# Performance work log

Hardware: AMD Instinct MI355X
Metric: run time of the kernel (lower is better)

The kernel has to match this reference:

```python
import jax, jax.numpy as jnp
import numpy as np

N_NODES = 100000


def gcn_conv(x, src, dst, W, b, num_nodes):
    # PyG GCNConv: add self-loops, symmetric normalization D^-1/2 (A+I) D^-1/2, then linear.
    loop = jnp.arange(num_nodes, dtype=src.dtype)
    s = jnp.concatenate([src, loop])
    d = jnp.concatenate([dst, loop])
    deg = jax.ops.segment_sum(jnp.ones_like(d, dtype=x.dtype), d, num_segments=num_nodes)
    dinv = jnp.where(deg > 0, jax.lax.rsqrt(deg), 0.0)
    norm = dinv[s] * dinv[d]                       # [E+N]
    h = x @ W                                      # [N, out]
    msg = h[s] * norm[:, None]                     # gather + scale
    out = jax.ops.segment_sum(msg, d, num_segments=num_nodes)  # scatter-add
    return out + b


def setup_inputs() -> dict:
    key = jax.random.key(0)
    k1, k2, k3, k4 = jax.random.split(key, 4)
    F_IN, HID, C = 165, 128, 2
    E = 3200000
    x = jax.random.normal(k1, (N_NODES, F_IN), dtype=jnp.float32)
    edge_index = jax.random.randint(k2, (2, E), 0, N_NODES, dtype=jnp.int64)
    W1 = jax.random.normal(k3, (F_IN, HID), dtype=jnp.float32) * (1.0 / np.sqrt(F_IN))
    b1 = jnp.zeros((HID,), dtype=jnp.float32)
    W2 = jax.random.normal(k4, (HID, C), dtype=jnp.float32) * (1.0 / np.sqrt(HID))
    b2 = jnp.zeros((C,), dtype=jnp.float32)
    return {"x": x, "edge_index": edge_index, "W1": W1, "b1": b1, "W2": W2, "b2": b2}


def reference(x, edge_index, W1, b1, W2, b2):
    src, dst = edge_index[0], edge_index[1]
    h = jax.nn.relu(gcn_conv(x, src, dst, W1, b1, N_NODES))
    # dropout is identity in eval mode (self.training=False)
    out = gcn_conv(h, src, dst, W2, b2, N_NODES)
    return out
```

## Files before the change

kernel.cpp:

```cpp
#include <hip/hip_runtime.h>

#define NN  100000
#define FIN 165
#define HID 128
#define NBUCK 391
#define CHUNK 8192
#define CAP   9216
#define KPAD 192
#define WS   196

typedef __attribute__((ext_vector_type(4))) float f32x4;
typedef __attribute__((ext_vector_type(8))) short short8;

#define OFF_DINV   0
#define OFF_H1     100352
#define OFF_Z      (OFF_H1 + NN * 64)
#define OFF_ROWPTR (OFF_Z + 2 * NN)
#define OFF_GBASE  (OFF_ROWPTR + 100352)
#define OFF_GCUR   (OFF_GBASE + 512)
#define OFF_BUCK   (OFF_GCUR + 512)
#define OFF_EDATA  (OFF_BUCK + NBUCK * CAP)
#define OFF_WTHI   (OFF_EDATA + 3200000)

__device__ __forceinline__ unsigned bf16rne(float f) {
    unsigned u = __float_as_uint(f);
    return (u + 0x7FFFu + ((u >> 16) & 1u)) >> 16;
}

__device__ __forceinline__ float2 bf2_to_f2(unsigned int u) {
    float2 r;
    r.x = __uint_as_float(u << 16);
    r.y = __uint_as_float(u & 0xffff0000u);
    return r;
}

__device__ __forceinline__ short8 ldfrag(const ushort* p) {
    union { uint2 u[2]; short8 s; } f;
    f.u[0] = *(const uint2*)p;
    f.u[1] = *(const uint2*)(p + 16);
    return f.s;
}

__global__ void k_wsplit(const float* __restrict__ W1, ushort* __restrict__ hi,
                         int* __restrict__ gcur) {
    int t = blockIdx.x * blockDim.x + threadIdx.x;
    if (t < 512) gcur[t] = t * CAP;
    if (t >= HID * KPAD) return;
    int ch = t / KPAD, k = t % KPAD;
    float v = (k < FIN) ? W1[k * HID + ch] : 0.0f;
    hi[ch * KPAD + k] = (ushort)bf16rne(v);
}

__global__ __launch_bounds__(1024) void k_bfill(const int* __restrict__ src,
        const int* __restrict__ dst, int* __restrict__ gcur,
        unsigned int* __restrict__ bucketed, int ne) {
    __shared__ int hist[NBUCK];
    __shared__ int lcur[NBUCK];
    for (int i = threadIdx.x; i < NBUCK; i += 1024) hist[i] = 0;
    __syncthreads();
    const int4* dst4 = (const int4*)dst;
    const int4* src4 = (const int4*)src;
    const int ne4 = ne >> 2;
    const int base4 = blockIdx.x * (CHUNK / 4);
#pragma unroll
    for (int it = 0; it < CHUNK / 4096; ++it) {
        int e4 = base4 + it * 1024 + threadIdx.x;
        if (e4 < ne4) {
            int4 v = dst4[e4];
            atomicAdd(&hist[v.x >> 8], 1);
            atomicAdd(&hist[v.y >> 8], 1);
            atomicAdd(&hist[v.z >> 8], 1);
            atomicAdd(&hist[v.w >> 8], 1);
        }
    }
    if (blockIdx.x == 0 && threadIdx.x < (ne & 3))
        atomicAdd(&hist[dst[(ne & ~3) + threadIdx.x] >> 8], 1);
    __syncthreads();
    for (int i = threadIdx.x; i < NBUCK; i += 1024) {
        int h = hist[i];
        lcur[i] = h ? atomicAdd(&gcur[i], h) : 0;
    }
    __syncthreads();
#define PUT(D, S)                                                            \
    {                                                                        \
        int b_ = (D) >> 8;                                                   \
        int pos_ = atomicAdd(&lcur[b_], 1);                                  \
        if (pos_ < (b_ + 1) * CAP)                                           \
            bucketed[pos_] = (unsigned)(S) | ((unsigned)((D) & 255) << 24);  \
    }
#pragma unroll
    for (int it = 0; it < CHUNK / 4096; ++it) {
        int e4 = base4 + it * 1024 + threadIdx.x;
        if (e4 < ne4) {
            int4 d4 = dst4[e4];
            int4 s4 = src4[e4];
            PUT(d4.x, s4.x);
            PUT(d4.y, s4.y);
            PUT(d4.z, s4.z);
            PUT(d4.w, s4.w);
        }
    }
    if (blockIdx.x == 0 && threadIdx.x < (ne & 3)) {
        int e = (ne & ~3) + threadIdx.x;
        PUT(dst[e], src[e]);
    }
#undef PUT
}

__global__ __launch_bounds__(512) void k_bscan(const int* __restrict__ gcur,
        int* __restrict__ gbase) {
    __shared__ int s[512];
    int tid = threadIdx.x;
    int c = 0;
    if (tid < NBUCK) {
        c = gcur[tid] - tid * CAP;
        c = min(c, CAP);
    }
    s[tid] = c;
    __syncthreads();
    for (int off = 1; off < 512; off <<= 1) {
        int t = (tid >= off) ? s[tid - off] : 0;
        __syncthreads();
        s[tid] += t;
        __syncthreads();
    }
    if (tid < NBUCK) gbase[tid] = s[tid] - c;
    if (tid == NBUCK - 1) gbase[NBUCK] = s[tid];
}

__global__ __launch_bounds__(512) void k_fused2(
        const float* __restrict__ x, const ushort* __restrict__ wthi,
        unsigned* __restrict__ h1, int n,
        const int* __restrict__ gbase, const unsigned int* __restrict__ bucketed,
        int* __restrict__ edata, int* __restrict__ rowptr,
        float* __restrict__ dinv) {
    __shared__ alignas(16) unsigned char smem[128 * WS * 2];

    if (blockIdx.x < NBUCK) {
        int* hist = (int*)smem;
        int* scan = hist + 256;
        int* lcur = scan + 256;
        const int b = blockIdx.x;
        const int tid = threadIdx.x;
        const int rbeg = b * CAP;
        const int wbeg = gbase[b], wend = gbase[b + 1];
        const int cnt = wend - wbeg;
        if (tid < 256) hist[tid] = 0;
        __syncthreads();
        for (int j = tid; j < cnt; j += 512)
            atomicAdd(&hist[bucketed[rbeg + j] >> 24], 1);
        __syncthreads();
        if (tid < 256) scan[tid] = hist[tid];
        __syncthreads();
        for (int off = 1; off < 256; off <<= 1) {
            int t = 0;
            if (tid < 256 && tid >= off) t = scan[tid - off];
            __syncthreads();
            if (tid < 256) scan[tid] += t;
            __syncthreads();
        }
        if (tid < 256) {
            int c = hist[tid];
            int excl = scan[tid] - c;
            int d = b * 256 + tid;
            if (d < n) {
                rowptr[d] = wbeg + excl;
                dinv[d] = rsqrtf((float)c + 1.0f);
            }
            lcur[tid] = wbeg + excl;
        }
        __syncthreads();
        for (int j = tid; j < cnt; j += 512) {
            unsigned p = bucketed[rbeg + j];
            int pos = atomicAdd(&lcur[p >> 24], 1);
            edata[pos] = (int)(p & 0x00FFFFFFu);
        }
        if (b == NBUCK - 1 && tid == 0) rowptr[n] = wend;
        return;
    }

    ushort* whi = (ushort*)smem;
    const int tid = threadIdx.x;
    const int node0 = (blockIdx.x - NBUCK) * 128;
    const int wv = tid >> 6, lane = tid & 63;
    const int r15 = lane & 15, g = lane >> 4;

    {
        int ch = tid >> 2, q = tid & 3;
        int gb = ch * KPAD + q * 48;
        int lb = ch * WS + q * 48;
#pragma unroll
        for (int j = 0; j < 12; ++j) {
            uint2 v = *(const uint2*)&wthi[gb + j * 4];
            *(uint2*)&whi[lb + j * 4] = v;
        }
    }

    const int row = node0 + wv * 16 + r15;
    const bool rowok = row < n;
    const float* xrow = x + (size_t)row * FIN;

    f32x4 acc[8];
#pragma unroll
    for (int ct = 0; ct < 8; ++ct) acc[ct] = (f32x4){0.f, 0.f, 0.f, 0.f};

    __syncthreads();

    for (int ks = 0; ks < 6; ++ks) {
        unsigned hh[8];
#pragma unroll
        for (int j = 0; j < 4; ++j) {
            int k0 = ks * 32 + 4 * g + j;
            int k1 = k0 + 16;
            float v0 = (rowok && k0 < FIN) ? xrow[k0] : 0.0f;
            float v1 = (rowok && k1 < FIN) ? xrow[k1] : 0.0f;
            hh[j]     = bf16rne(v0);
            hh[4 + j] = bf16rne(v1);
        }
        union { unsigned u[4]; short8 s; } A;
        A.u[0] = hh[0] | (hh[1] << 16);
        A.u[1] = hh[2] | (hh[3] << 16);
        A.u[2] = hh[4] | (hh[5] << 16);
        A.u[3] = hh[6] | (hh[7] << 16);
#pragma unroll
        for (int ct = 0; ct < 8; ++ct) {
            short8 Bh = ldfrag(&whi[(ct * 16 + r15) * WS + ks * 32 + 4 * g]);
            acc[ct] = __builtin_amdgcn_mfma_f32_16x16x32_bf16(A.s, Bh, acc[ct], 0, 0, 0);
        }
    }

#pragma unroll
    for (int ct = 0; ct < 4; ++ct) {
#pragma unroll
        for (int r = 0; r < 4; ++r) {
            int node = node0 + wv * 16 + 4 * g + r;
            if (node < n) {
                unsigned p = bf16rne(acc[ct][r]) | (bf16rne(acc[ct + 4][r]) << 16);
                h1[node * 64 + ct * 16 + r15] = p;
            }
        }
    }
}

__global__ __launch_bounds__(256) void k_agg_fused(const int* __restrict__ rowptr,
        const int* __restrict__ edata, const unsigned int* __restrict__ h1,
        const float* __restrict__ dinv, const float* __restrict__ b1,
        const float* __restrict__ W2, float* __restrict__ z, int n) {
    const int wid  = (blockIdx.x * blockDim.x + threadIdx.x) >> 6;
    const int lane = threadIdx.x & 63;
    if (wid >= n) return;
    const int d = wid;
    const int beg = rowptr[d], end = rowptr[d + 1];
    const float di = dinv[d];
    const int grp = lane >> 4;
    const int sl  = lane & 15;

    float ax0, ax1, ax2, ax3, ay0, ay1, ay2, ay3;
    {
        uint4 hv = *(const uint4*)&h1[d * 64 + sl * 4];
        float nm = (grp == 0) ? di * di : 0.0f;
        float2 f0 = bf2_to_f2(hv.x), f1 = bf2_to_f2(hv.y);
        float2 f2 = bf2_to_f2(hv.z), f3 = bf2_to_f2(hv.w);
        ax0 = f0.x * nm; ay0 = f0.y * nm;
        ax1 = f1.x * nm; ay1 = f1.y * nm;
        ax2 = f2.x * nm; ay2 = f2.y * nm;
        ax3 = f3.x * nm; ay3 = f3.y * nm;
    }

#define PRELOAD(JB)                                                          \
    {                                                                        \
        int i0 = (JB) + grp, i1 = (JB) + 4 + grp,                            \
            i2 = (JB) + 8 + grp, i3 = (JB) + 12 + grp;                       \
        int c0 = min(i0, end - 1), c1 = min(i1, end - 1);                    \
        int c2 = min(i2, end - 1), c3 = min(i3, end - 1);                    \
        s0 = edata[c0]; s1 = edata[c1]; s2 = edata[c2]; s3 = edata[c3];      \
        m0 = (i0 < end) ? dinv[s0] * di : 0.0f;                              \
        m1 = (i1 < end) ? dinv[s1] * di : 0.0f;                              \
        m2 = (i2 < end) ? dinv[s2] * di : 0.0f;                              \
        m3 = (i3 < end) ? dinv[s3] * di : 0.0f;                              \
    }
#define ACC(G, NM)                                                           \
    {                                                                        \
        float2 f;                                                            \
        f = bf2_to_f2((G).x); ax0 = fmaf(f.x, (NM), ax0); ay0 = fmaf(f.y, (NM), ay0); \
        f = bf2_to_f2((G).y); ax1 = fmaf(f.x, (NM), ax1); ay1 = fmaf(f.y, (NM), ay1); \
        f = bf2_to_f2((G).z); ax2 = fmaf(f.x, (NM), ax2); ay2 = fmaf(f.y, (NM), ay2); \
        f = bf2_to_f2((G).w); ax3 = fmaf(f.x, (NM), ax3); ay3 = fmaf(f.y, (NM), ay3); \
    }

    if (beg < end) {
        int s0, s1, s2, s3;
        float m0, m1, m2, m3;
        PRELOAD(beg);
        for (int j = beg; j < end; j += 16) {
            uint4 g0 = *(const uint4*)&h1[s0 * 64 + sl * 4];
            uint4 g1 = *(const uint4*)&h1[s1 * 64 + sl * 4];
            uint4 g2 = *(const uint4*)&h1[s2 * 64 + sl * 4];
            uint4 g3 = *(const uint4*)&h1[s3 * 64 + sl * 4];
            float w0 = m0, w1 = m1, w2 = m2, w3 = m3;
            int jn = j + 16;
            if (jn < end) PRELOAD(jn);
            ACC(g0, w0); ACC(g1, w1); ACC(g2, w2); ACC(g3, w3);
        }
    }
#undef PRELOAD
#undef ACC

    ax0 += __shfl_xor(ax0, 16, 64); ax0 += __shfl_xor(ax0, 32, 64);
    ax1 += __shfl_xor(ax1, 16, 64); ax1 += __shfl_xor(ax1, 32, 64);
    ax2 += __shfl_xor(ax2, 16, 64); ax2 += __shfl_xor(ax2, 32, 64);
    ax3 += __shfl_xor(ax3, 16, 64); ax3 += __shfl_xor(ax3, 32, 64);
    ay0 += __shfl_xor(ay0, 16, 64); ay0 += __shfl_xor(ay0, 32, 64);
    ay1 += __shfl_xor(ay1, 16, 64); ay1 += __shfl_xor(ay1, 32, 64);
    ay2 += __shfl_xor(ay2, 16, 64); ay2 += __shfl_xor(ay2, 32, 64);
    ay3 += __shfl_xor(ay3, 16, 64); ay3 += __shfl_xor(ay3, 32, 64);
    const int c = sl * 4;
    float4 bA = *(const float4*)&b1[c];
    float4 bB = *(const float4*)&b1[c + 64];
    float v00 = ax0 + bA.x; v00 = v00 > 0.f ? v00 : 0.f;
    float v01 = ax1 + bA.y; v01 = v01 > 0.f ? v01 : 0.f;
    float v02 = ax2 + bA.z; v02 = v02 > 0.f ? v02 : 0.f;
    float v03 = ax3 + bA.w; v03 = v03 > 0.f ? v03 : 0.f;
    float v10 = ay0 + bB.x; v10 = v10 > 0.f ? v10 : 0.f;
    float v11 = ay1 + bB.y; v11 = v11 > 0.f ? v11 : 0.f;
    float v12 = ay2 + bB.z; v12 = v12 > 0.f ? v12 : 0.f;
    float v13 = ay3 + bB.w; v13 = v13 > 0.f ? v13 : 0.f;
    float4 wA0 = *(const float4*)&W2[c * 2];
    float4 wA1 = *(const float4*)&W2[c * 2 + 4];
    float4 wB0 = *(const float4*)&W2[(c + 64) * 2];
    float4 wB1 = *(const float4*)&W2[(c + 64) * 2 + 4];
    float p0 = v00 * wA0.x + v01 * wA0.z + v02 * wA1.x + v03 * wA1.z
             + v10 * wB0.x + v11 * wB0.z + v12 * wB1.x + v13 * wB1.z;
    float p1 = v00 * wA0.y + v01 * wA0.w + v02 * wA1.y + v03 * wA1.w
             + v10 * wB0.y + v11 * wB0.w + v12 * wB1.y + v13 * wB1.w;
#pragma unroll
    for (int m = 8; m >= 1; m >>= 1) {
        p0 += __shfl_xor(p0, m, 64);
        p1 += __shfl_xor(p1, m, 64);
    }
    if (lane == 0) *(float2*)&z[d * 2] = make_float2(p0, p1);
}

__global__ __launch_bounds__(256) void k_out(const int* __restrict__ rowptr,
        const int* __restrict__ edata, const float* __restrict__ z,
        const float* __restrict__ dinv, const float* __restrict__ b2,
        float* __restrict__ out, int n) {
    int g = (blockIdx.x * blockDim.x + threadIdx.x) >> 4;
    int l = threadIdx.x & 15;
    if (g >= n) return;
    int beg = rowptr[g], end = rowptr[g + 1];
    float di = dinv[g];
    float o0 = 0.0f, o1 = 0.0f;
    for (int j = beg + l; j < end; j += 16) {
        int s = edata[j];
        float nm = dinv[s] * di;
        float2 zs = *(const float2*)&z[s * 2];
        o0 = fmaf(zs.x, nm, o0);
        o1 = fmaf(zs.y, nm, o1);
    }
#pragma unroll
    for (int m = 8; m >= 1; m >>= 1) {
        o0 += __shfl_xor(o0, m, 16);
        o1 += __shfl_xor(o1, m, 16);
    }
    if (l == 0) {
        float2 zd = *(const float2*)&z[g * 2];
        float s2 = di * di;
        out[g * 2]     = fmaf(zd.x, s2, b2[0]) + o0;
        out[g * 2 + 1] = fmaf(zd.y, s2, b2[1]) + o1;
    }
}

extern "C" void kernel_launch(void* const* d_in, const int* in_sizes, int n_in,
                              void* d_out, int out_size, void* d_ws, size_t ws_size,
                              hipStream_t stream) {
    const float* x  = (const float*)d_in[0];
    const int*   ei = (const int*)d_in[1];
    const float* W1 = (const float*)d_in[2];
    const float* b1 = (const float*)d_in[3];
    const float* W2 = (const float*)d_in[4];
    const float* b2 = (const float*)d_in[5];
    float* out = (float*)d_out;

    const int n  = in_sizes[0] / FIN;
    const int ne = in_sizes[1] / 2;
    const int* src = ei;
    const int* dst = ei + ne;

    float* ws     = (float*)d_ws;
    float* dinv   = ws + OFF_DINV;
    unsigned int* h1 = (unsigned int*)(ws + OFF_H1);
    float* z      = ws + OFF_Z;
    int*   rowptr = (int*)(ws + OFF_ROWPTR);
    int*   gbase  = (int*)(ws + OFF_GBASE);
    int*   gcur   = (int*)(ws + OFF_GCUR);
    unsigned int* bucketed = (unsigned int*)(ws + OFF_BUCK);
    int*   edata  = (int*)(ws + OFF_EDATA);
    ushort* wthi  = (ushort*)(ws + OFF_WTHI);

    const int nchb  = (ne + CHUNK - 1) / CHUNK;
    const int ngemm = (n + 127) / 128;

    k_wsplit<<<(HID * KPAD + 255) / 256, 256, 0, stream>>>(W1, wthi, gcur);
    k_bfill<<<nchb, 1024, 0, stream>>>(src, dst, gcur, bucketed, ne);
    k_bscan<<<1, 512, 0, stream>>>(gcur, gbase);
    k_fused2<<<NBUCK + ngemm, 512, 0, stream>>>(x, wthi, h1, n,
                                                gbase, bucketed, edata, rowptr, dinv);
    k_agg_fused<<<((size_t)n * 64 + 255) / 256, 256, 0, stream>>>(
        rowptr, edata, h1, dinv, b1, W2, z, n);
    k_out<<<(n * 16 + 255) / 256, 256, 0, stream>>>(rowptr, edata, z, dinv, b2, out, n);
}
```

Before: 227.5 us.

## Drop bucket scan kernel, use per-bucket padded CSR and deeper gather prefetch

Removes the single-block bucket prefix-scan kernel by keeping edges in padded per-bucket regions and storing separate row begin and end arrays, so the CSR build no longer needs a global scan or one extra launch. The bucket-fill kernel now uses a fixed count of 256 persistent blocks that each loop over a contiguous slice, which cuts global atomics on the bucket cursors. The layer-1 aggregation gathers 32 neighbours per iteration instead of 16, giving more loads in flight per wave. The costs are a larger edata buffer, extra row-end reads, and more registers in the aggregation kernel.

```diff
diff --git a/kernel.cpp b/kernel.cpp
--- a/kernel.cpp
+++ b/kernel.cpp
@@ -4,10 +4,10 @@
 #define FIN 165
 #define HID 128
 #define NBUCK 391
-#define CHUNK 8192
 #define CAP   9216
 #define KPAD 192
 #define WS   196
+#define NBLK 256
 
 typedef __attribute__((ext_vector_type(4))) float f32x4;
 typedef __attribute__((ext_vector_type(8))) short short8;
@@ -15,12 +15,12 @@
 #define OFF_DINV   0
 #define OFF_H1     100352
 #define OFF_Z      (OFF_H1 + NN * 64)
-#define OFF_ROWPTR (OFF_Z + 2 * NN)
-#define OFF_GBASE  (OFF_ROWPTR + 100352)
-#define OFF_GCUR   (OFF_GBASE + 512)
+#define OFF_ROWB   (OFF_Z + 2 * NN)
+#define OFF_ROWE   (OFF_ROWB + 100352)
+#define OFF_GCUR   (OFF_ROWE + 100352)
 #define OFF_BUCK   (OFF_GCUR + 512)
 #define OFF_EDATA  (OFF_BUCK + NBUCK * CAP)
-#define OFF_WTHI   (OFF_EDATA + 3200000)
+#define OFF_WTHI   (OFF_EDATA + NBUCK * CAP)
 
 __device__ __forceinline__ unsigned bf16rne(float f) {
     unsigned u = __float_as_uint(f);
@@ -61,17 +61,15 @@
     const int4* dst4 = (const int4*)dst;
     const int4* src4 = (const int4*)src;
     const int ne4 = ne >> 2;
-    const int base4 = blockIdx.x * (CHUNK / 4);
-#pragma unroll
-    for (int it = 0; it < CHUNK / 4096; ++it) {
-        int e4 = base4 + it * 1024 + threadIdx.x;
-        if (e4 < ne4) {
-            int4 v = dst4[e4];
-            atomicAdd(&hist[v.x >> 8], 1);
-            atomicAdd(&hist[v.y >> 8], 1);
-            atomicAdd(&hist[v.z >> 8], 1);
-            atomicAdd(&hist[v.w >> 8], 1);
-        }
+    const int per4 = (ne4 + NBLK - 1) / NBLK;
+    const int b0 = blockIdx.x * per4;
+    const int b1 = min(ne4, b0 + per4);
+    for (int e4 = b0 + (int)threadIdx.x; e4 < b1; e4 += 1024) {
+        int4 v = dst4[e4];
+        atomicAdd(&hist[v.x >> 8], 1);
+        atomicAdd(&hist[v.y >> 8], 1);
+        atomicAdd(&hist[v.z >> 8], 1);
+        atomicAdd(&hist[v.w >> 8], 1);
     }
     if (blockIdx.x == 0 && threadIdx.x < (ne & 3))
         atomicAdd(&hist[dst[(ne & ~3) + threadIdx.x] >> 8], 1);
@@ -88,17 +86,13 @@
         if (pos_ < (b_ + 1) * CAP)                                           \
             bucketed[pos_] = (unsigned)(S) | ((unsigned)((D) & 255) << 24);  \
     }
-#pragma unroll
-    for (int it = 0; it < CHUNK / 4096; ++it) {
-        int e4 = base4 + it * 1024 + threadIdx.x;
-        if (e4 < ne4) {
-            int4 d4 = dst4[e4];
-            int4 s4 = src4[e4];
-            PUT(d4.x, s4.x);
-            PUT(d4.y, s4.y);
-            PUT(d4.z, s4.z);
-            PUT(d4.w, s4.w);
-        }
+    for (int e4 = b0 + (int)threadIdx.x; e4 < b1; e4 += 1024) {
+        int4 d4 = dst4[e4];
+        int4 s4 = src4[e4];
+        PUT(d4.x, s4.x);
+        PUT(d4.y, s4.y);
+        PUT(d4.z, s4.z);
+        PUT(d4.w, s4.w);
     }
     if (blockIdx.x == 0 && threadIdx.x < (ne & 3)) {
         int e = (ne & ~3) + threadIdx.x;
@@ -107,33 +101,12 @@
 #undef PUT
 }
 
-__global__ __launch_bounds__(512) void k_bscan(const int* __restrict__ gcur,
-        int* __restrict__ gbase) {
-    __shared__ int s[512];
-    int tid = threadIdx.x;
-    int c = 0;
-    if (tid < NBUCK) {
-        c = gcur[tid] - tid * CAP;
-        c = min(c, CAP);
-    }
-    s[tid] = c;
-    __syncthreads();
-    for (int off = 1; off < 512; off <<= 1) {
-        int t = (tid >= off) ? s[tid - off] : 0;
-        __syncthreads();
-        s[tid] += t;
-        __syncthreads();
-    }
-    if (tid < NBUCK) gbase[tid] = s[tid] - c;
-    if (tid == NBUCK - 1) gbase[NBUCK] = s[tid];
-}
-
 __global__ __launch_bounds__(512) void k_fused2(
         const float* __restrict__ x, const ushort* __restrict__ wthi,
         unsigned* __restrict__ h1, int n,
-        const int* __restrict__ gbase, const unsigned int* __restrict__ bucketed,
-        int* __restrict__ edata, int* __restrict__ rowptr,
-        float* __restrict__ dinv) {
+        const int* __restrict__ gcur, const unsigned int* __restrict__ bucketed,
+        int* __restrict__ edata, int* __restrict__ rowbeg,
+        int* __restrict__ rowend, float* __restrict__ dinv) {
     __shared__ alignas(16) unsigned char smem[128 * WS * 2];
 
     if (blockIdx.x < NBUCK) {
@@ -143,8 +116,7 @@
         const int b = blockIdx.x;
         const int tid = threadIdx.x;
         const int rbeg = b * CAP;
-        const int wbeg = gbase[b], wend = gbase[b + 1];
-        const int cnt = wend - wbeg;
+        const int cnt = min(gcur[b] - rbeg, CAP);
         if (tid < 256) hist[tid] = 0;
         __syncthreads();
         for (int j = tid; j < cnt; j += 512)
@@ -164,10 +136,11 @@
             int excl = scan[tid] - c;
             int d = b * 256 + tid;
             if (d < n) {
-                rowptr[d] = wbeg + excl;
+                rowbeg[d] = rbeg + excl;
+                rowend[d] = rbeg + excl + c;
                 dinv[d] = rsqrtf((float)c + 1.0f);
             }
-            lcur[tid] = wbeg + excl;
+            lcur[tid] = rbeg + excl;
         }
         __syncthreads();
         for (int j = tid; j < cnt; j += 512) {
@@ -175,7 +148,6 @@
             int pos = atomicAdd(&lcur[p >> 24], 1);
             edata[pos] = (int)(p & 0x00FFFFFFu);
         }
-        if (b == NBUCK - 1 && tid == 0) rowptr[n] = wend;
         return;
     }
 
@@ -242,15 +214,16 @@
     }
 }
 
-__global__ __launch_bounds__(256) void k_agg_fused(const int* __restrict__ rowptr,
-        const int* __restrict__ edata, const unsigned int* __restrict__ h1,
-        const float* __restrict__ dinv, const float* __restrict__ b1,
-        const float* __restrict__ W2, float* __restrict__ z, int n) {
+__global__ __launch_bounds__(256) void k_agg_fused(const int* __restrict__ rowbeg,
+        const int* __restrict__ rowend, const int* __restrict__ edata,
+        const unsigned int* __restrict__ h1, const float* __restrict__ dinv,
+        const float* __restrict__ b1, const float* __restrict__ W2,
+        float* __restrict__ z, int n) {
     const int wid  = (blockIdx.x * blockDim.x + threadIdx.x) >> 6;
     const int lane = threadIdx.x & 63;
     if (wid >= n) return;
     const int d = wid;
-    const int beg = rowptr[d], end = rowptr[d + 1];
+    const int beg = rowbeg[d], end = rowend[d];
     const float di = dinv[d];
     const int grp = lane >> 4;
     const int sl  = lane & 15;
@@ -267,17 +240,15 @@
         ax3 = f3.x * nm; ay3 = f3.y * nm;
     }
 
-#define PRELOAD(JB)                                                          \
+#define PRELOAD32(JB)                                                        \
     {                                                                        \
-        int i0 = (JB) + grp, i1 = (JB) + 4 + grp,                            \
-            i2 = (JB) + 8 + grp, i3 = (JB) + 12 + grp;                       \
-        int c0 = min(i0, end - 1), c1 = min(i1, end - 1);                    \
-        int c2 = min(i2, end - 1), c3 = min(i3, end - 1);                    \
-        s0 = edata[c0]; s1 = edata[c1]; s2 = edata[c2]; s3 = edata[c3];      \
-        m0 = (i0 < end) ? dinv[s0] * di : 0.0f;                              \
-        m1 = (i1 < end) ? dinv[s1] * di : 0.0f;                              \
-        m2 = (i2 < end) ? dinv[s2] * di : 0.0f;                              \
-        m3 = (i3 < end) ? dinv[s3] * di : 0.0f;                              \
+        _Pragma("unroll")                                                    \
+        for (int q = 0; q < 8; ++q) {                                        \
+            int i_ = (JB) + q * 4 + grp;                                     \
+            int c_ = min(i_, end - 1);                                       \
+            sA[q] = edata[c_];                                               \
+            mA[q] = (i_ < end) ? dinv[sA[q]] * di : 0.0f;                    \
+        }                                                                    \
     }
 #define ACC(G, NM)                                                           \
     {                                                                        \
@@ -289,21 +260,24 @@
     }
 
     if (beg < end) {
-        int s0, s1, s2, s3;
-        float m0, m1, m2, m3;
-        PRELOAD(beg);
-        for (int j = beg; j < end; j += 16) {
-            uint4 g0 = *(const uint4*)&h1[s0 * 64 + sl * 4];
-            uint4 g1 = *(const uint4*)&h1[s1 * 64 + sl * 4];
-            uint4 g2 = *(const uint4*)&h1[s2 * 64 + sl * 4];
-            uint4 g3 = *(const uint4*)&h1[s3 * 64 + sl * 4];
-            float w0 = m0, w1 = m1, w2 = m2, w3 = m3;
-            int jn = j + 16;
-            if (jn < end) PRELOAD(jn);
-            ACC(g0, w0); ACC(g1, w1); ACC(g2, w2); ACC(g3, w3);
-        }
-    }
-#undef PRELOAD
+        int sA[8];
+        float mA[8];
+        PRELOAD32(beg);
+        for (int j = beg; j < end; j += 32) {
+            uint4 gv[8];
+#pragma unroll
+            for (int q = 0; q < 8; ++q)
+                gv[q] = *(const uint4*)&h1[sA[q] * 64 + sl * 4];
+            float wv_[8];
+#pragma unroll
+            for (int q = 0; q < 8; ++q) wv_[q] = mA[q];
+            int jn = j + 32;
+            if (jn < end) PRELOAD32(jn);
+#pragma unroll
+            for (int q = 0; q < 8; ++q) ACC(gv[q], wv_[q]);
+        }
+    }
+#undef PRELOAD32
 #undef ACC
 
     ax0 += __shfl_xor(ax0, 16, 64); ax0 += __shfl_xor(ax0, 32, 64);
@@ -341,14 +315,14 @@
     if (lane == 0) *(float2*)&z[d * 2] = make_float2(p0, p1);
 }
 
-__global__ __launch_bounds__(256) void k_out(const int* __restrict__ rowptr,
-        const int* __restrict__ edata, const float* __restrict__ z,
-        const float* __restrict__ dinv, const float* __restrict__ b2,
-        float* __restrict__ out, int n) {
+__global__ __launch_bounds__(256) void k_out(const int* __restrict__ rowbeg,
+        const int* __restrict__ rowend, const int* __restrict__ edata,
+        const float* __restrict__ z, const float* __restrict__ dinv,
+        const float* __restrict__ b2, float* __restrict__ out, int n) {
     int g = (blockIdx.x * blockDim.x + threadIdx.x) >> 4;
     int l = threadIdx.x & 15;
     if (g >= n) return;
-    int beg = rowptr[g], end = rowptr[g + 1];
+    int beg = rowbeg[g], end = rowend[g];
     float di = dinv[g];
     float o0 = 0.0f, o1 = 0.0f;
     for (int j = beg + l; j < end; j += 16) {
@@ -391,22 +365,22 @@
     float* dinv   = ws + OFF_DINV;
     unsigned int* h1 = (unsigned int*)(ws + OFF_H1);
     float* z      = ws + OFF_Z;
-    int*   rowptr = (int*)(ws + OFF_ROWPTR);
-    int*   gbase  = (int*)(ws + OFF_GBASE);
+    int*   rowbeg = (int*)(ws + OFF_ROWB);
+    int*   rowend = (int*)(ws + OFF_ROWE);
     int*   gcur   = (int*)(ws + OFF_GCUR);
     unsigned int* bucketed = (unsigned int*)(ws + OFF_BUCK);
     int*   edata  = (int*)(ws + OFF_EDATA);
     ushort* wthi  = (ushort*)(ws + OFF_WTHI);
 
-    const int nchb  = (ne + CHUNK - 1) / CHUNK;
     const int ngemm = (n + 127) / 128;
 
     k_wsplit<<<(HID * KPAD + 255) / 256, 256, 0, stream>>>(W1, wthi, gcur);
-    k_bfill<<<nchb, 1024, 0, stream>>>(src, dst, gcur, bucketed, ne);
-    k_bscan<<<1, 512, 0, stream>>>(gcur, gbase);
+    k_bfill<<<NBLK, 1024, 0, stream>>>(src, dst, gcur, bucketed, ne);
     k_fused2<<<NBUCK + ngemm, 512, 0, stream>>>(x, wthi, h1, n,
-                                                gbase, bucketed, edata, rowptr, dinv);
+                                                gcur, bucketed, edata,
+                                                rowbeg, rowend, dinv);
     k_agg_fused<<<((size_t)n * 64 + 255) / 256, 256, 0, stream>>>(
-        rowptr, edata, h1, dinv, b1, W2, z, n);
-    k_out<<<(n * 16 + 255) / 256, 256, 0, stream>>>(rowptr, edata, z, dinv, b2, out, n);
-}
+        rowbeg, rowend, edata, h1, dinv, b1, W2, z, n);
+    k_out<<<(n * 16 + 255) / 256, 256, 0, stream>>>(rowbeg, rowend, edata,
+                                                    z, dinv, b2, out, n);
+}
```

Result: slower. 270.9 us (+19.1%).
